# Optimization experiments

Measured on AMD Instinct MI355X. Metric: run time of the kernel, lower is better.

## Reference

```python
import jax, jax.numpy as jnp
import numpy as np
import math

D = 256      # d_model
HEADS = 8
PTS = 4      # num_points
L = 6        # num_layers
FF = 1024    # dim_feedforward
B = 8
HS, WS = 100, 100  # feature map -> N = 10000
HD = D // HEADS


def setup_inputs() -> dict:
    key = jax.random.key(0)
    ks = jax.random.split(key, 8)
    w = lambda k, shape, s: jax.random.normal(k, shape, jnp.float32) * s
    z = lambda *shape: jnp.zeros(shape, jnp.float32)
    return {
        "src": jax.random.normal(ks[0], (B, HS * WS, D), jnp.float32),
        "Wv": w(ks[1], (L, D, D), 0.02), "bv": z(L, D),
        "Woff": w(ks[2], (L, D, HEADS * PTS * 2), 0.01), "boff": z(L, HEADS * PTS * 2),
        "Wa": w(ks[3], (L, D, HEADS * PTS), 0.02), "ba": z(L, HEADS * PTS),
        "Wo": w(ks[4], (L, D, D), 0.02), "bo": z(L, D),
        "W1": w(ks[5], (L, D, FF), 0.02), "b1": z(L, FF),
        "W2": w(ks[6], (L, FF, D), 0.02), "b2": z(L, D),
        "g1": jnp.ones((L, D)), "be1": z(L, D),
        "g2": jnp.ones((L, D)), "be2": z(L, D),
        "H": HS, "W": WS,
    }


def pos_encoding_2d(d_model, H, W):
    # standard 2D sine encoding: first half of channels encode y, second half x
    half = d_model // 2
    freqs = jnp.exp(-math.log(10000.0) * jnp.arange(0, half, 2, dtype=jnp.float32) / half)
    ya = jnp.arange(H, dtype=jnp.float32)[:, None] * freqs[None, :]
    xa = jnp.arange(W, dtype=jnp.float32)[:, None] * freqs[None, :]
    pe_y = jnp.stack([jnp.sin(ya), jnp.cos(ya)], -1).reshape(H, half)
    pe_x = jnp.stack([jnp.sin(xa), jnp.cos(xa)], -1).reshape(W, half)
    pe = jnp.concatenate([
        jnp.broadcast_to(pe_y[:, None, :], (H, W, half)),
        jnp.broadcast_to(pe_x[None, :, :], (H, W, half))], -1)
    return pe.reshape(H * W, d_model)


def layer_norm(x, g, b, eps=1e-5):
    m = x.mean(-1, keepdims=True)
    v = ((x - m) ** 2).mean(-1, keepdims=True)
    return (x - m) * jax.lax.rsqrt(v + eps) * g + b


def deform_attn(q, Wv, bv, Woff, boff, Wa, ba, Wo, bo, H, W):
    # single-scale Deformable-DETR attention; q: [B, N, D], N = H*W
    Bq, N, _ = q.shape
    v = (q @ Wv + bv).reshape(Bq, N, HEADS, HD)
    off = (q @ Woff + boff).reshape(Bq, N, HEADS, PTS, 2)          # (dx, dy) in pixels
    attn = jax.nn.softmax((q @ Wa + ba).reshape(Bq, N, HEADS, PTS), axis=-1)
    # reference points: normalized grid cell centers
    ys, xs = jnp.meshgrid(jnp.arange(H, dtype=jnp.float32),
                          jnp.arange(W, dtype=jnp.float32), indexing='ij')
    ref = jnp.stack([(xs.reshape(-1) + 0.5) / W, (ys.reshape(-1) + 0.5) / H], -1)  # [N,2]
    loc = ref[None, :, None, None, :] + off / jnp.array([W, H], jnp.float32)       # [B,N,h,P,2]
    # pixel coords, align_corners=False; border padding via clamping
    px = loc[..., 0] * W - 0.5
    py = loc[..., 1] * H - 0.5
    x0 = jnp.floor(px); y0 = jnp.floor(py)
    wx = px - x0; wy = py - y0
    x0i = jnp.clip(x0.astype(jnp.int32), 0, W - 1); x1i = jnp.clip(x0i + 1, 0, W - 1)
    y0i = jnp.clip(y0.astype(jnp.int32), 0, H - 1); y1i = jnp.clip(y0i + 1, 0, H - 1)
    vbh = v.transpose(0, 2, 1, 3).reshape(Bq * HEADS, N, HD)       # [B*h, N, hd]
    flat = lambda yi, xi: (yi * W + xi).transpose(0, 2, 1, 3).reshape(Bq * HEADS, N * PTS)
    gather = jax.vmap(lambda val, idx: val[idx])                   # [B*h, N*P, hd]
    wxr = wx.transpose(0, 2, 1, 3).reshape(Bq * HEADS, N * PTS, 1)
    wyr = wy.transpose(0, 2, 1, 3).reshape(Bq * HEADS, N * PTS, 1)
    s = (gather(vbh, flat(y0i, x0i)) * (1 - wxr) * (1 - wyr)
         + gather(vbh, flat(y0i, x1i)) * wxr * (1 - wyr)
         + gather(vbh, flat(y1i, x0i)) * (1 - wxr) * wyr
         + gather(vbh, flat(y1i, x1i)) * wxr * wyr)
    s = s.reshape(Bq, HEADS, N, PTS, HD)
    out = jnp.einsum('bhnp,bhnpd->bhnd', attn.transpose(0, 2, 1, 3), s)
    out = out.transpose(0, 2, 1, 3).reshape(Bq, N, D)
    return out @ Wo + bo


def reference(src, Wv, bv, Woff, boff, Wa, ba, Wo, bo, W1, b1, W2, b2,
              g1, be1, g2, be2, H, W):
    x = src + pos_encoding_2d(D, H, W)[None]
    for i in range(L):
        a = deform_attn(x, Wv[i], bv[i], Woff[i], boff[i], Wa[i], ba[i], Wo[i], bo[i], H, W)
        x = layer_norm(x + a, g1[i], be1[i])
        h = jax.nn.gelu(x @ W1[i] + b1[i], approximate=False)
        x = layer_norm(x + (h @ W2[i] + b2[i]), g2[i], be2[i])
    return x
```

## Files before the change

### kernel.cpp

```cpp
#include <hip/hip_runtime.h>
#include <hip/hip_bf16.h>
#include <math.h>

#define Bq   8
#define NPix 10000
#define HH   100
#define WW   100
#define Dm   256
#define NH   8
#define HD   32
#define PTS  4
#define FFd  1024
#define Lnum 6
#define Mrows (Bq * NPix)

typedef short bf16x8 __attribute__((ext_vector_type(8)));
typedef short short4v __attribute__((ext_vector_type(4)));
typedef float f32x4 __attribute__((ext_vector_type(4)));

__device__ __forceinline__ float bf2f(unsigned short u) {
    return __uint_as_float(((unsigned)u) << 16);
}
__device__ __forceinline__ unsigned short f2bf(float f) {
    unsigned x = __float_as_uint(f);
    return (unsigned short)((x + 0x7fffu + ((x >> 16) & 1u)) >> 16);
}

__global__ __launch_bounds__(256) void pos_add_kernel(
    const float* __restrict__ src, float* __restrict__ x, short* __restrict__ xb)
{
    int idx = blockIdx.x * 256 + threadIdx.x;
    int c = idx & (Dm - 1);
    int n = (idx >> 8) % NPix;
    int cc = c;
    float coord;
    if (c < 128) { coord = (float)(n / WW); }
    else         { coord = (float)(n % WW); cc = c - 128; }
    int j = cc >> 1;
    float f = __expf(-logf(10000.0f) * (2.0f * (float)j) / 128.0f);
    float arg = coord * f;
    float pe = (cc & 1) ? cosf(arg) : sinf(arg);
    float val = src[idx] + pe;
    x[idx] = val;
    xb[idx] = (short)f2bf(val);
}

__global__ __launch_bounds__(256) void repack_kernel(
    const float* __restrict__ W, short* __restrict__ Wt,
    int K, int N, int outLstride, int nOff)
{
    __shared__ float t[64][65];
    int l  = blockIdx.z;
    int k0 = blockIdx.y * 64, n0 = blockIdx.x * 64;
    const float* Wl = W + (size_t)l * K * N;
    for (int i = threadIdx.x; i < 64 * 64; i += 256) {
        int kk = i >> 6, nn = i & 63;
        float val = 0.0f;
        if (k0 + kk < K && n0 + nn < N) val = Wl[(size_t)(k0 + kk) * N + (n0 + nn)];
        t[kk][nn] = val;
    }
    __syncthreads();
    for (int i = threadIdx.x; i < 64 * 64; i += 256) {
        int nn = i >> 6, kk = i & 63;
        if (n0 + nn < N && k0 + kk < K)
            Wt[(size_t)l * outLstride + (size_t)(nOff + n0 + nn) * K + (k0 + kk)]
                = (short)f2bf(t[kk][nn]);
    }
}

__global__ void bcat_kernel(const float* __restrict__ bv,
                            const float* __restrict__ boff,
                            const float* __restrict__ ba,
                            float* __restrict__ bcat)
{
    int l = blockIdx.x, c = threadIdx.x;
    float v;
    if (c < 256)      v = bv[l * 256 + c];
    else if (c < 320) v = boff[l * 64 + (c - 256)];
    else              v = ba[l * 32 + (c - 320)];
    bcat[l * 352 + c] = v;
}

template<bool GELU, int MODE>
__global__ __launch_bounds__(256) void gemm_mfma_kernel(
    const short* __restrict__ A, const short* __restrict__ Bt,
    const float* __restrict__ bias, void* __restrict__ Cv,
    float* __restrict__ C2,
    int M, int K, int Nc, int ldc)
{
    __shared__ short As[128 * 64];
    __shared__ short Bs[128 * 64];
    const int tid = threadIdx.x;

    int nwg  = gridDim.x * gridDim.y;
    int orig = blockIdx.y * gridDim.x + blockIdx.x;
    int xcd  = orig & 7, pos = orig >> 3;
    int q = nwg >> 3, r = nwg & 7;
    int flat = (xcd < r ? xcd * (q + 1) : r * (q + 1) + (xcd - r) * q) + pos;
    const int bm = (flat / gridDim.x) * 128;
    const int bn = (flat % gridDim.x) * 128;

    const int w = tid >> 6, l = tid & 63;
    const int wr = (w >> 1) * 64, wc = (w & 1) * 64;

    f32x4 acc[4][4];
    #pragma unroll
    for (int m = 0; m < 4; ++m)
        #pragma unroll
        for (int n = 0; n < 4; ++n)
            #pragma unroll
            for (int j = 0; j < 4; ++j) acc[m][n][j] = 0.0f;

    const int rl = tid >> 3;
    const int cl = tid & 7;
    const int lr = l & 15, lq = l >> 4;

    for (int k0 = 0; k0 < K; k0 += 64) {
        #pragma unroll
        for (int p = 0; p < 4; ++p) {
            int row = p * 32 + rl;
            int sc  = cl ^ (row & 7);
            int ga  = bm + row; if (ga > M - 1) ga = M - 1;
            __builtin_amdgcn_global_load_lds((const void*)(A + (size_t)ga * K + k0 + sc * 8),
                (void*)&As[(p * 32 + w * 8) * 64], 16, 0, 0);
            int gb = bn + row; if (gb > Nc - 1) gb = Nc - 1;
            __builtin_amdgcn_global_load_lds((const void*)(Bt + (size_t)gb * K + k0 + sc * 8),
                (void*)&Bs[(p * 32 + w * 8) * 64], 16, 0, 0);
        }
        __syncthreads();

        #pragma unroll
        for (int ks = 0; ks < 2; ++ks) {
            bf16x8 af[4], bfr[4];
            #pragma unroll
            for (int m = 0; m < 4; ++m) {
                int row = wr + m * 16 + lr;
                int ch  = (ks * 4 + lq) ^ (row & 7);
                af[m] = *(const bf16x8*)&As[row * 64 + ch * 8];
            }
            #pragma unroll
            for (int n = 0; n < 4; ++n) {
                int row = wc + n * 16 + lr;
                int ch  = (ks * 4 + lq) ^ (row & 7);
                bfr[n] = *(const bf16x8*)&Bs[row * 64 + ch * 8];
            }
            #pragma unroll
            for (int m = 0; m < 4; ++m)
                #pragma unroll
                for (int n = 0; n < 4; ++n)
                    acc[m][n] = __builtin_amdgcn_mfma_f32_16x16x32_bf16(
                        af[m], bfr[n], acc[m][n], 0, 0, 0);
        }
        __syncthreads();
    }

    #pragma unroll
    for (int m = 0; m < 4; ++m) {
        int row0 = bm + wr + m * 16 + lq * 4;
        #pragma unroll
        for (int n = 0; n < 4; ++n) {
            int col = bn + wc + n * 16 + lr;
            if (col >= Nc) continue;
            float bi = bias[col];
            #pragma unroll
            for (int j = 0; j < 4; ++j) {
                int rr = row0 + j;
                if (rr >= M) continue;
                float val = acc[m][n][j] + bi;
                if (GELU)
                    val = 0.5f * val * (1.0f + erff(val * 0.70710678118654752f));
                if (MODE == 1) {
                    ((short*)Cv)[(size_t)rr * ldc + col] = (short)f2bf(val);
                } else {
                    if (col < 256)
                        ((short*)Cv)[(size_t)rr * 256 + col] = (short)f2bf(val);
                    else
                        C2[(size_t)rr * 96 + (col - 256)] = val;
                }
            }
        }
    }
}

__global__ __launch_bounds__(256) void gemm_ln_kernel(
    const short* __restrict__ A, const short* __restrict__ Bt,
    const float* __restrict__ bias,
    const float* __restrict__ gw, const float* __restrict__ bw,
    float* __restrict__ x, short* __restrict__ xb,
    int M, int K)
{
    __shared__ short As[64 * 64];
    __shared__ short Bs[256 * 64];
    const int tid = threadIdx.x;
    const int bm = blockIdx.x * 64;
    const int w = tid >> 6, l = tid & 63;
    const int rl = tid >> 3, cl = tid & 7;
    const int lr = l & 15, lq = l >> 4;

    f32x4 acc[16];
    #pragma unroll
    for (int n = 0; n < 16; ++n)
        #pragma unroll
        for (int j = 0; j < 4; ++j) acc[n][j] = 0.0f;

    for (int k0 = 0; k0 < K; k0 += 64) {
        #pragma unroll
        for (int p = 0; p < 2; ++p) {
            int row = p * 32 + rl;
            int sc  = cl ^ (row & 7);
            int ga  = bm + row; if (ga > M - 1) ga = M - 1;
            __builtin_amdgcn_global_load_lds((const void*)(A + (size_t)ga * K + k0 + sc * 8),
                (void*)&As[(p * 32 + w * 8) * 64], 16, 0, 0);
        }
        #pragma unroll
        for (int p = 0; p < 8; ++p) {
            int row = p * 32 + rl;
            int sc  = cl ^ (row & 7);
            __builtin_amdgcn_global_load_lds((const void*)(Bt + (size_t)row * K + k0 + sc * 8),
                (void*)&Bs[(p * 32 + w * 8) * 64], 16, 0, 0);
        }
        __syncthreads();

        #pragma unroll
        for (int ks = 0; ks < 2; ++ks) {
            int arow = w * 16 + lr;
            bf16x8 af = *(const bf16x8*)&As[arow * 64 + (((ks * 4 + lq) ^ (arow & 7))) * 8];
            #pragma unroll
            for (int hb = 0; hb < 2; ++hb) {
                bf16x8 bfr[8];
                #pragma unroll
                for (int i = 0; i < 8; ++i) {
                    int brow = (hb * 8 + i) * 16 + lr;
                    bfr[i] = *(const bf16x8*)&Bs[brow * 64 + (((ks * 4 + lq) ^ (brow & 7))) * 8];
                }
                #pragma unroll
                for (int i = 0; i < 8; ++i)
                    acc[hb * 8 + i] = __builtin_amdgcn_mfma_f32_16x16x32_bf16(
                        af, bfr[i], acc[hb * 8 + i], 0, 0, 0);
            }
        }
        __syncthreads();
    }

    float bi[16];
    #pragma unroll
    for (int n = 0; n < 16; ++n) bi[n] = bias[n * 16 + lr];

    #pragma unroll
    for (int j = 0; j < 4; ++j) {
        int rr = bm + w * 16 + lq * 4 + j;
        if (rr < M) {
            float tmp[16];
            float sum = 0.0f;
            #pragma unroll
            for (int n = 0; n < 16; ++n) {
                int c = n * 16 + lr;
                float val = acc[n][j] + bi[n] + x[(size_t)rr * 256 + c];
                tmp[n] = val;
                sum += val;
            }
            #pragma unroll
            for (int o = 8; o >= 1; o >>= 1) sum += __shfl_xor(sum, o);
            float mean = sum * (1.0f / 256.0f);
            float vs = 0.0f;
            #pragma unroll
            for (int n = 0; n < 16; ++n) {
                float d = tmp[n] - mean;
                vs += d * d;
            }
            #pragma unroll
            for (int o = 8; o >= 1; o >>= 1) vs += __shfl_xor(vs, o);
            float rstd = rsqrtf(vs * (1.0f / 256.0f) + 1e-5f);
            #pragma unroll
            for (int n = 0; n < 16; ++n) {
                int c = n * 16 + lr;
                float ov = (tmp[n] - mean) * rstd * gw[c] + bw[c];
                x[(size_t)rr * 256 + c] = ov;
                xb[(size_t)rr * 256 + c] = (short)f2bf(ov);
            }
        }
    }
}

__global__ __launch_bounds__(256) void deform_attn_kernel(
    const short* __restrict__ v, const float* __restrict__ comb,
    short* __restrict__ outs)
{
    int g  = blockIdx.x * 16 + (threadIdx.x >> 4);
    int d2 = threadIdx.x & 15;
    int bn = g >> 3, h = g & 7;
    int n  = bn % NPix;
    int row = n / WW, col = n % WW;
    int base_v = (bn / NPix) * NPix;

    const float* cb = comb + (size_t)bn * 96;
    float l0 = cb[64 + h * 4 + 0], l1 = cb[64 + h * 4 + 1];
    float l2 = cb[64 + h * 4 + 2], l3 = cb[64 + h * 4 + 3];
    float mx = fmaxf(fmaxf(l0, l1), fmaxf(l2, l3));
    float e0 = __expf(l0 - mx), e1 = __expf(l1 - mx);
    float e2 = __expf(l2 - mx), e3 = __expf(l3 - mx);
    float inv = 1.0f / (e0 + e1 + e2 + e3);
    float aw[4] = {e0 * inv, e1 * inv, e2 * inv, e3 * inv};

    float acc0 = 0.0f, acc1 = 0.0f;
    size_t chb = (size_t)h * HD + d2 * 2;
    #pragma unroll
    for (int p = 0; p < 4; ++p) {
        float dx = cb[h * 8 + p * 2 + 0];
        float dy = cb[h * 8 + p * 2 + 1];
        float px = (float)col + dx;
        float py = (float)row + dy;
        float x0f = floorf(px), y0f = floorf(py);
        float wx = px - x0f, wy = py - y0f;
        int x0i = min(max((int)x0f, 0), WW - 1);
        int y0i = min(max((int)y0f, 0), HH - 1);
        int x1i = min(x0i + 1, WW - 1);
        int y1i = min(y0i + 1, HH - 1);
        unsigned u00 = *(const unsigned*)&v[(size_t)(base_v + y0i * WW + x0i) * Dm + chb];
        unsigned u01 = *(const unsigned*)&v[(size_t)(base_v + y0i * WW + x1i) * Dm + chb];
        unsigned u10 = *(const unsigned*)&v[(size_t)(base_v + y1i * WW + x0i) * Dm + chb];
        unsigned u11 = *(const unsigned*)&v[(size_t)(base_v + y1i * WW + x1i) * Dm + chb];
        float w00 = (1.0f - wx) * (1.0f - wy), w01 = wx * (1.0f - wy);
        float w10 = (1.0f - wx) * wy,          w11 = wx * wy;
        float s0 = bf2f((unsigned short)u00) * w00 + bf2f((unsigned short)u01) * w01
                 + bf2f((unsigned short)u10) * w10 + bf2f((unsigned short)u11) * w11;
        float s1 = bf2f((unsigned short)(u00 >> 16)) * w00 + bf2f((unsigned short)(u01 >> 16)) * w01
                 + bf2f((unsigned short)(u10 >> 16)) * w10 + bf2f((unsigned short)(u11 >> 16)) * w11;
        acc0 = fmaf(aw[p], s0, acc0);
        acc1 = fmaf(aw[p], s1, acc1);
    }
    unsigned outw = (unsigned)f2bf(acc0) | ((unsigned)f2bf(acc1) << 16);
    *(unsigned*)&outs[(size_t)bn * Dm + chb] = outw;
}

extern "C" void kernel_launch(void* const* d_in, const int* in_sizes, int n_in,
                              void* d_out, int out_size, void* d_ws, size_t ws_size,
                              hipStream_t stream)
{
    const float* src  = (const float*)d_in[0];
    const float* Wv   = (const float*)d_in[1];
    const float* bv   = (const float*)d_in[2];
    const float* Woff = (const float*)d_in[3];
    const float* boff = (const float*)d_in[4];
    const float* Wa   = (const float*)d_in[5];
    const float* ba   = (const float*)d_in[6];
    const float* Wo   = (const float*)d_in[7];
    const float* bo   = (const float*)d_in[8];
    const float* W1   = (const float*)d_in[9];
    const float* b1   = (const float*)d_in[10];
    const float* W2   = (const float*)d_in[11];
    const float* b2   = (const float*)d_in[12];
    const float* g1   = (const float*)d_in[13];
    const float* be1  = (const float*)d_in[14];
    const float* g2   = (const float*)d_in[15];
    const float* be2  = (const float*)d_in[16];

    float* x = (float*)d_out;

    char* cur = (char*)d_ws;
    auto take = [&](size_t bytes) { char* p = cur; cur += (bytes + 255) & ~(size_t)255; return p; };
    short* WcatT = (short*)take((size_t)Lnum * 352 * Dm * 2);
    short* WoT   = (short*)take((size_t)Lnum * Dm * Dm * 2);
    short* W1T   = (short*)take((size_t)Lnum * Dm * FFd * 2);
    short* W2T   = (short*)take((size_t)Lnum * FFd * Dm * 2);
    float* bcat  = (float*)take((size_t)Lnum * 352 * 4);
    short* xb    = (short*)take((size_t)Mrows * Dm * 2);
    size_t fixedB = (size_t)(cur - (char*)d_ws);

    const size_t perRowB = 512 + 512 + 384 + 2048;
    int k = 8;
    while (k > 1 && fixedB + (size_t)k * NPix * perRowB > ws_size) k >>= 1;
    if (fixedB + (size_t)k * NPix * perRowB > ws_size) return;
    const int CM = k * NPix;
    const int nChunks = Bq / k;

    short* v    = (short*)take((size_t)CM * Dm * 2);
    short* sbuf = (short*)take((size_t)CM * Dm * 2);
    float* comb = (float*)take((size_t)CM * 96 * 4);
    short* h    = (short*)take((size_t)CM * FFd * 2);

    repack_kernel<<<dim3(4, 4, Lnum),  256, 0, stream>>>(Wv,   WcatT, Dm,  Dm,  352 * Dm,   0);
    repack_kernel<<<dim3(1, 4, Lnum),  256, 0, stream>>>(Woff, WcatT, Dm,  64,  352 * Dm, 256);
    repack_kernel<<<dim3(1, 4, Lnum),  256, 0, stream>>>(Wa,   WcatT, Dm,  32,  352 * Dm, 320);
    repack_kernel<<<dim3(4, 4, Lnum),  256, 0, stream>>>(Wo,   WoT,   Dm,  Dm,  Dm * Dm,    0);
    repack_kernel<<<dim3(16, 4, Lnum), 256, 0, stream>>>(W1,   W1T,   Dm,  FFd, Dm * FFd,   0);
    repack_kernel<<<dim3(4, 16, Lnum), 256, 0, stream>>>(W2,   W2T,   FFd, Dm,  FFd * Dm,   0);
    bcat_kernel<<<Lnum, 352, 0, stream>>>(bv, boff, ba, bcat);

    pos_add_kernel<<<Mrows, 256, 0, stream>>>(src, x, xb);

    const int gy   = (CM + 127) / 128;
    const int gLN  = (CM + 63) / 64;

    for (int l = 0; l < Lnum; ++l) {
        const short* WcatT_l = WcatT + (size_t)l * 352 * Dm;
        const short* WoT_l   = WoT   + (size_t)l * Dm * Dm;
        const short* W1T_l   = W1T   + (size_t)l * Dm * FFd;
        const short* W2T_l   = W2T   + (size_t)l * FFd * Dm;

        for (int c = 0; c < nChunks; ++c) {
            size_t rowOff = (size_t)c * CM;
            float* xc  = x  + rowOff * Dm;
            short* xbc = xb + rowOff * Dm;

            gemm_mfma_kernel<false, 2><<<dim3(3, gy), 256, 0, stream>>>(
                xbc, WcatT_l, bcat + l * 352, v, comb, CM, Dm, 352, 0);
            deform_attn_kernel<<<CM / 2, 256, 0, stream>>>(v, comb, sbuf);
            gemm_ln_kernel<<<gLN, 256, 0, stream>>>(
                sbuf, WoT_l, bo + l * Dm, g1 + l * Dm, be1 + l * Dm, xc, xbc, CM, Dm);
            gemm_mfma_kernel<true, 1><<<dim3(8, gy), 256, 0, stream>>>(
                xbc, W1T_l, b1 + l * FFd, h, nullptr, CM, Dm, FFd, FFd);
            gemm_ln_kernel<<<gLN, 256, 0, stream>>>(
                h, W2T_l, b2 + l * Dm, g2 + l * Dm, be2 + l * Dm, xc, xbc, CM, FFd);
        }
    }
}
```

Before: 2.706 ms.

## Fuse FFN up-projection, GELU, down-projection and LayerNorm into one kernel

Replaces the separate W1 GEMM+GELU kernel and the W2 GEMM+LayerNorm kernel with a single kernel. Each 64-row block computes the 1024-wide hidden activation in four 256-column strips kept in LDS and immediately accumulates them into the W2 output, so the bf16 hidden tensor never goes to global memory. This removes the hidden-buffer write and read and one launch per chunk, and frees workspace for larger chunks. The cost is heavy LDS use (about 96KB per block), which limits occupancy, and weight tiles reloaded per 64-row block with little overlap between loads and MFMA.

```diff
diff --git a/kernel.cpp b/kernel.cpp
--- a/kernel.cpp
+++ b/kernel.cpp
@@ -245,6 +245,180 @@
     float bi[16];
     #pragma unroll
     for (int n = 0; n < 16; ++n) bi[n] = bias[n * 16 + lr];
+
+    #pragma unroll
+    for (int j = 0; j < 4; ++j) {
+        int rr = bm + w * 16 + lq * 4 + j;
+        if (rr < M) {
+            float tmp[16];
+            float sum = 0.0f;
+            #pragma unroll
+            for (int n = 0; n < 16; ++n) {
+                int c = n * 16 + lr;
+                float val = acc[n][j] + bi[n] + x[(size_t)rr * 256 + c];
+                tmp[n] = val;
+                sum += val;
+            }
+            #pragma unroll
+            for (int o = 8; o >= 1; o >>= 1) sum += __shfl_xor(sum, o);
+            float mean = sum * (1.0f / 256.0f);
+            float vs = 0.0f;
+            #pragma unroll
+            for (int n = 0; n < 16; ++n) {
+                float d = tmp[n] - mean;
+                vs += d * d;
+            }
+            #pragma unroll
+            for (int o = 8; o >= 1; o >>= 1) vs += __shfl_xor(vs, o);
+            float rstd = rsqrtf(vs * (1.0f / 256.0f) + 1e-5f);
+            #pragma unroll
+            for (int n = 0; n < 16; ++n) {
+                int c = n * 16 + lr;
+                float ov = (tmp[n] - mean) * rstd * gw[c] + bw[c];
+                x[(size_t)rr * 256 + c] = ov;
+                xb[(size_t)rr * 256 + c] = (short)f2bf(ov);
+            }
+        }
+    }
+}
+
+__global__ __launch_bounds__(256) void ffn_ln_kernel(
+    const short* __restrict__ A,
+    const short* __restrict__ W1T,
+    const short* __restrict__ W2T,
+    const float* __restrict__ b1, const float* __restrict__ b2,
+    const float* __restrict__ gw, const float* __restrict__ bw,
+    float* __restrict__ x, short* __restrict__ xb,
+    int M)
+{
+    __shared__ short As[64 * 256];
+    __shared__ short hL[64 * 256];
+    __shared__ short Wst[256 * 64];
+    const int tid = threadIdx.x;
+    const int bm = blockIdx.x * 64;
+    const int w = tid >> 6, l = tid & 63;
+    const int lr = l & 15, lq = l >> 4;
+
+    #pragma unroll
+    for (int p = 0; p < 8; ++p) {
+        int s = p * 256 + tid;
+        int row = s >> 5, cs = s & 31;
+        int c = cs ^ (row & 7);
+        int ga = bm + row; if (ga > M - 1) ga = M - 1;
+        __builtin_amdgcn_global_load_lds((const void*)(A + (size_t)ga * 256 + c * 8),
+            (void*)&As[(size_t)(p * 256 + w * 64) * 8], 16, 0, 0);
+    }
+
+    f32x4 acc[16];
+    #pragma unroll
+    for (int n = 0; n < 16; ++n)
+        #pragma unroll
+        for (int j = 0; j < 4; ++j) acc[n][j] = 0.0f;
+
+    const int srow = tid >> 3;
+
+    for (int strip = 0; strip < 4; ++strip) {
+        f32x4 hacc[16];
+        #pragma unroll
+        for (int n = 0; n < 16; ++n)
+            #pragma unroll
+            for (int j = 0; j < 4; ++j) hacc[n][j] = 0.0f;
+
+        const short* W1s = W1T + (size_t)(strip * 256) * 256;
+        for (int kc = 0; kc < 4; ++kc) {
+            __syncthreads();
+            #pragma unroll
+            for (int p = 0; p < 8; ++p) {
+                int s = p * 256 + tid;
+                int row = s >> 3, cs = s & 7;
+                int c = cs ^ (row & 7);
+                __builtin_amdgcn_global_load_lds(
+                    (const void*)(W1s + (size_t)row * 256 + kc * 64 + c * 8),
+                    (void*)&Wst[(size_t)(p * 256 + w * 64) * 8], 16, 0, 0);
+            }
+            __syncthreads();
+
+            #pragma unroll
+            for (int ks = 0; ks < 2; ++ks) {
+                int arow = w * 16 + lr;
+                int ac = (kc * 8 + ks * 4 + lq) ^ (arow & 7);
+                bf16x8 xf = *(const bf16x8*)&As[arow * 256 + ac * 8];
+                #pragma unroll
+                for (int hb = 0; hb < 2; ++hb) {
+                    bf16x8 wf[8];
+                    #pragma unroll
+                    for (int i = 0; i < 8; ++i) {
+                        int wrow = (hb * 8 + i) * 16 + lr;
+                        wf[i] = *(const bf16x8*)&Wst[wrow * 64 + (((ks * 4 + lq) ^ (wrow & 7))) * 8];
+                    }
+                    #pragma unroll
+                    for (int i = 0; i < 8; ++i)
+                        hacc[hb * 8 + i] = __builtin_amdgcn_mfma_f32_16x16x32_bf16(
+                            wf[i], xf, hacc[hb * 8 + i], 0, 0, 0);
+                }
+            }
+        }
+
+        {
+            int hrow = w * 16 + lr;
+            #pragma unroll
+            for (int n = 0; n < 16; ++n) {
+                float4 b1v = *(const float4*)(b1 + strip * 256 + n * 16 + lq * 4);
+                float o0 = hacc[n][0] + b1v.x;
+                float o1 = hacc[n][1] + b1v.y;
+                float o2 = hacc[n][2] + b1v.z;
+                float o3 = hacc[n][3] + b1v.w;
+                o0 = 0.5f * o0 * (1.0f + erff(o0 * 0.70710678118654752f));
+                o1 = 0.5f * o1 * (1.0f + erff(o1 * 0.70710678118654752f));
+                o2 = 0.5f * o2 * (1.0f + erff(o2 * 0.70710678118654752f));
+                o3 = 0.5f * o3 * (1.0f + erff(o3 * 0.70710678118654752f));
+                unsigned lo = (unsigned)f2bf(o0) | ((unsigned)f2bf(o1) << 16);
+                unsigned hi = (unsigned)f2bf(o2) | ((unsigned)f2bf(o3) << 16);
+                int col = n * 16 + lq * 4;
+                int slot = (col >> 3) ^ (hrow & 7);
+                unsigned long long val = ((unsigned long long)hi << 32) | (unsigned long long)lo;
+                *(unsigned long long*)((char*)hL + (size_t)hrow * 512 + slot * 16 + (col & 7) * 2) = val;
+            }
+        }
+
+        for (int kc = 0; kc < 4; ++kc) {
+            __syncthreads();
+            #pragma unroll
+            for (int p = 0; p < 8; ++p) {
+                int s = p * 256 + tid;
+                int row = s >> 3, cs = s & 7;
+                int c = cs ^ (row & 7);
+                __builtin_amdgcn_global_load_lds(
+                    (const void*)(W2T + (size_t)row * 1024 + strip * 256 + kc * 64 + c * 8),
+                    (void*)&Wst[(size_t)(p * 256 + w * 64) * 8], 16, 0, 0);
+            }
+            __syncthreads();
+
+            #pragma unroll
+            for (int ks = 0; ks < 2; ++ks) {
+                int hrow = w * 16 + lr;
+                int hc = (kc * 8 + ks * 4 + lq) ^ (hrow & 7);
+                bf16x8 hf = *(const bf16x8*)&hL[hrow * 256 + hc * 8];
+                #pragma unroll
+                for (int hb = 0; hb < 2; ++hb) {
+                    bf16x8 wf[8];
+                    #pragma unroll
+                    for (int i = 0; i < 8; ++i) {
+                        int wrow = (hb * 8 + i) * 16 + lr;
+                        wf[i] = *(const bf16x8*)&Wst[wrow * 64 + (((ks * 4 + lq) ^ (wrow & 7))) * 8];
+                    }
+                    #pragma unroll
+                    for (int i = 0; i < 8; ++i)
+                        acc[hb * 8 + i] = __builtin_amdgcn_mfma_f32_16x16x32_bf16(
+                            hf, wf[i], acc[hb * 8 + i], 0, 0, 0);
+                }
+            }
+        }
+    }
+
+    float bi[16];
+    #pragma unroll
+    for (int n = 0; n < 16; ++n) bi[n] = b2[n * 16 + lr];
 
     #pragma unroll
     for (int j = 0; j < 4; ++j) {
@@ -367,7 +541,7 @@
     short* xb    = (short*)take((size_t)Mrows * Dm * 2);
     size_t fixedB = (size_t)(cur - (char*)d_ws);
 
-    const size_t perRowB = 512 + 512 + 384 + 2048;
+    const size_t perRowB = 512 + 512 + 384;
     int k = 8;
     while (k > 1 && fixedB + (size_t)k * NPix * perRowB > ws_size) k >>= 1;
     if (fixedB + (size_t)k * NPix * perRowB > ws_size) return;
@@ -377,7 +551,6 @@
     short* v    = (short*)take((size_t)CM * Dm * 2);
     short* sbuf = (short*)take((size_t)CM * Dm * 2);
     float* comb = (float*)take((size_t)CM * 96 * 4);
-    short* h    = (short*)take((size_t)CM * FFd * 2);
 
     repack_kernel<<<dim3(4, 4, Lnum),  256, 0, stream>>>(Wv,   WcatT, Dm,  Dm,  352 * Dm,   0);
     repack_kernel<<<dim3(1, 4, Lnum),  256, 0, stream>>>(Woff, WcatT, Dm,  64,  352 * Dm, 256);
@@ -389,8 +562,8 @@
 
     pos_add_kernel<<<Mrows, 256, 0, stream>>>(src, x, xb);
 
-    const int gy   = (CM + 127) / 128;
-    const int gLN  = (CM + 63) / 64;
+    const int gy  = (CM + 127) / 128;
+    const int gLN = (CM + 63) / 64;
 
     for (int l = 0; l < Lnum; ++l) {
         const short* WcatT_l = WcatT + (size_t)l * 352 * Dm;
@@ -408,10 +581,9 @@
             deform_attn_kernel<<<CM / 2, 256, 0, stream>>>(v, comb, sbuf);
             gemm_ln_kernel<<<gLN, 256, 0, stream>>>(
                 sbuf, WoT_l, bo + l * Dm, g1 + l * Dm, be1 + l * Dm, xc, xbc, CM, Dm);
-            gemm_mfma_kernel<true, 1><<<dim3(8, gy), 256, 0, stream>>>(
-                xbc, W1T_l, b1 + l * FFd, h, nullptr, CM, Dm, FFd, FFd);
-            gemm_ln_kernel<<<gLN, 256, 0, stream>>>(
-                h, W2T_l, b2 + l * Dm, g2 + l * Dm, be2 + l * Dm, xc, xbc, CM, FFd);
-        }
-    }
-}
+            ffn_ln_kernel<<<gLN, 256, 0, stream>>>(
+                xbc, W1T_l, W2T_l, b1 + l * FFd, b2 + l * Dm,
+                g2 + l * Dm, be2 + l * Dm, xc, xbc, CM);
+        }
+    }
+}
```

Result: slower. 3.035 ms (+12.2%).

## Replace W1/Wo/W2 GEMMs with persistent double-buffered 256x256 tile kernel

Applied to the files above, without the earlier changes.

Adds a persistent 512-thread GEMM kernel with 256x256 output tiles, double-buffered LDS staging that prefetches the next k-chunk or next tile, and XCD-aware tile assignment. It serves the Wo and W2 projections with a fused residual+LayerNorm epilogue that reduces across waves through shared memory, and the W1 projection with a GELU epilogue. The aim is more operand reuse per tile and load/compute overlap. In exchange it uses 128KB+ of LDS and large accumulator register arrays, which limits occupancy and can leave many CUs idle when there are few 256-row tiles.

```diff
diff --git a/kernel.cpp b/kernel.cpp
--- a/kernel.cpp
+++ b/kernel.cpp
@@ -15,7 +15,6 @@
 #define Mrows (Bq * NPix)
 
 typedef short bf16x8 __attribute__((ext_vector_type(8)));
-typedef short short4v __attribute__((ext_vector_type(4)));
 typedef float f32x4 __attribute__((ext_vector_type(4)));
 
 __device__ __forceinline__ float bf2f(unsigned short u) {
@@ -81,12 +80,11 @@
     bcat[l * 352 + c] = v;
 }
 
-template<bool GELU, int MODE>
 __global__ __launch_bounds__(256) void gemm_mfma_kernel(
     const short* __restrict__ A, const short* __restrict__ Bt,
-    const float* __restrict__ bias, void* __restrict__ Cv,
+    const float* __restrict__ bias, short* __restrict__ Cv,
     float* __restrict__ C2,
-    int M, int K, int Nc, int ldc)
+    int M, int K, int Nc)
 {
     __shared__ short As[128 * 64];
     __shared__ short Bs[128 * 64];
@@ -167,116 +165,206 @@
                 int rr = row0 + j;
                 if (rr >= M) continue;
                 float val = acc[m][n][j] + bi;
-                if (GELU)
-                    val = 0.5f * val * (1.0f + erff(val * 0.70710678118654752f));
-                if (MODE == 1) {
-                    ((short*)Cv)[(size_t)rr * ldc + col] = (short)f2bf(val);
-                } else {
-                    if (col < 256)
-                        ((short*)Cv)[(size_t)rr * 256 + col] = (short)f2bf(val);
-                    else
-                        C2[(size_t)rr * 96 + (col - 256)] = val;
-                }
-            }
-        }
-    }
-}
-
-__global__ __launch_bounds__(256) void gemm_ln_kernel(
+                if (col < 256)
+                    Cv[(size_t)rr * 256 + col] = (short)f2bf(val);
+                else
+                    C2[(size_t)rr * 96 + (col - 256)] = val;
+            }
+        }
+    }
+}
+
+template<int EPI>
+__global__ __launch_bounds__(512, 2) void gemm2_kernel(
     const short* __restrict__ A, const short* __restrict__ Bt,
     const float* __restrict__ bias,
+    short* __restrict__ C, int ldc,
+    float* __restrict__ x, short* __restrict__ xb,
     const float* __restrict__ gw, const float* __restrict__ bw,
-    float* __restrict__ x, short* __restrict__ xb,
-    int M, int K)
-{
-    __shared__ short As[64 * 64];
-    __shared__ short Bs[256 * 64];
+    int M, int K, int Nc, int nTilesM, int nTilesN)
+{
+    __shared__ short As[2][256 * 64];
+    __shared__ short Bs[2][256 * 64];
+    __shared__ float sredS[4][256];
+    __shared__ float sredM[256];
+    __shared__ float sredR[256];
+
     const int tid = threadIdx.x;
-    const int bm = blockIdx.x * 64;
-    const int w = tid >> 6, l = tid & 63;
-    const int rl = tid >> 3, cl = tid & 7;
-    const int lr = l & 15, lq = l >> 4;
-
-    f32x4 acc[16];
-    #pragma unroll
-    for (int n = 0; n < 16; ++n)
+    const int w   = tid >> 6;
+    const int l   = tid & 63;
+    const int lr  = l & 15, lq = l >> 4;
+    const int wr  = (w >> 2) * 128;
+    const int wcg = w & 3;
+    const int wc  = wcg * 64;
+
+    const int nT = nTilesM * nTilesN;
+    const int kIters = K >> 6;
+
+    const int nwg = gridDim.x;
+    {
+    }
+    int orig = blockIdx.x;
+    int xcd = orig & 7, pos = orig >> 3;
+    int q8 = nwg >> 3, r8 = nwg & 7;
+    int b0 = (xcd < r8 ? xcd * (q8 + 1) : r8 * (q8 + 1) + (xcd - r8) * q8) + pos;
+
+    auto stage = [&](int buf, int t, int kc) {
+        int tm = t / nTilesN, tn = t - tm * nTilesN;
         #pragma unroll
-        for (int j = 0; j < 4; ++j) acc[n][j] = 0.0f;
-
-    for (int k0 = 0; k0 < K; k0 += 64) {
+        for (int p = 0; p < 4; ++p) {
+            int s = p * 512 + tid;
+            int row = s >> 3, cs = s & 7;
+            int c = cs ^ (row & 7);
+            int ga = tm * 256 + row; if (ga > M - 1) ga = M - 1;
+            __builtin_amdgcn_global_load_lds(
+                (const void*)(A + (size_t)ga * K + kc * 64 + c * 8),
+                (void*)&As[buf][(p * 512 + w * 64) * 8], 16, 0, 0);
+            int gb = tn * 256 + row;
+            __builtin_amdgcn_global_load_lds(
+                (const void*)(Bt + (size_t)gb * K + kc * 64 + c * 8),
+                (void*)&Bs[buf][(p * 512 + w * 64) * 8], 16, 0, 0);
+        }
+    };
+
+    f32x4 acc[8][4];
+    int cur = 0;
+    int t = b0;
+    if (t < nT) stage(0, t, 0);
+
+    for (; t < nT; t += nwg) {
+        const int tm = t / nTilesN, tn = t - tm * nTilesN;
+
         #pragma unroll
-        for (int p = 0; p < 2; ++p) {
-            int row = p * 32 + rl;
-            int sc  = cl ^ (row & 7);
-            int ga  = bm + row; if (ga > M - 1) ga = M - 1;
-            __builtin_amdgcn_global_load_lds((const void*)(A + (size_t)ga * K + k0 + sc * 8),
-                (void*)&As[(p * 32 + w * 8) * 64], 16, 0, 0);
-        }
-        #pragma unroll
-        for (int p = 0; p < 8; ++p) {
-            int row = p * 32 + rl;
-            int sc  = cl ^ (row & 7);
-            __builtin_amdgcn_global_load_lds((const void*)(Bt + (size_t)row * K + k0 + sc * 8),
-                (void*)&Bs[(p * 32 + w * 8) * 64], 16, 0, 0);
-        }
-        __syncthreads();
-
-        #pragma unroll
-        for (int ks = 0; ks < 2; ++ks) {
-            int arow = w * 16 + lr;
-            bf16x8 af = *(const bf16x8*)&As[arow * 64 + (((ks * 4 + lq) ^ (arow & 7))) * 8];
-            #pragma unroll
-            for (int hb = 0; hb < 2; ++hb) {
-                bf16x8 bfr[8];
-                #pragma unroll
-                for (int i = 0; i < 8; ++i) {
-                    int brow = (hb * 8 + i) * 16 + lr;
-                    bfr[i] = *(const bf16x8*)&Bs[brow * 64 + (((ks * 4 + lq) ^ (brow & 7))) * 8];
+        for (int m = 0; m < 8; ++m)
+            #pragma unroll
+            for (int n = 0; n < 4; ++n)
+                #pragma unroll
+                for (int j = 0; j < 4; ++j) acc[m][n][j] = 0.0f;
+
+        for (int kc = 0; kc < kIters; ++kc) {
+            __syncthreads();
+            int nt2 = t, nk = kc + 1;
+            if (nk == kIters) { nt2 = t + nwg; nk = 0; }
+            if (nt2 < nT) stage(cur ^ 1, nt2, nk);
+
+            #pragma unroll
+            for (int ks = 0; ks < 2; ++ks) {
+                bf16x8 af[8], bfr[4];
+                #pragma unroll
+                for (int m = 0; m < 8; ++m) {
+                    int row = wr + m * 16 + lr;
+                    int ch  = (ks * 4 + lq) ^ (row & 7);
+                    af[m] = *(const bf16x8*)&As[cur][row * 64 + ch * 8];
                 }
                 #pragma unroll
-                for (int i = 0; i < 8; ++i)
-                    acc[hb * 8 + i] = __builtin_amdgcn_mfma_f32_16x16x32_bf16(
-                        af, bfr[i], acc[hb * 8 + i], 0, 0, 0);
-            }
-        }
-        __syncthreads();
-    }
-
-    float bi[16];
-    #pragma unroll
-    for (int n = 0; n < 16; ++n) bi[n] = bias[n * 16 + lr];
-
-    #pragma unroll
-    for (int j = 0; j < 4; ++j) {
-        int rr = bm + w * 16 + lq * 4 + j;
-        if (rr < M) {
-            float tmp[16];
-            float sum = 0.0f;
-            #pragma unroll
-            for (int n = 0; n < 16; ++n) {
-                int c = n * 16 + lr;
-                float val = acc[n][j] + bi[n] + x[(size_t)rr * 256 + c];
-                tmp[n] = val;
-                sum += val;
-            }
-            #pragma unroll
-            for (int o = 8; o >= 1; o >>= 1) sum += __shfl_xor(sum, o);
-            float mean = sum * (1.0f / 256.0f);
-            float vs = 0.0f;
-            #pragma unroll
-            for (int n = 0; n < 16; ++n) {
-                float d = tmp[n] - mean;
-                vs += d * d;
-            }
-            #pragma unroll
-            for (int o = 8; o >= 1; o >>= 1) vs += __shfl_xor(vs, o);
-            float rstd = rsqrtf(vs * (1.0f / 256.0f) + 1e-5f);
-            #pragma unroll
-            for (int n = 0; n < 16; ++n) {
-                int c = n * 16 + lr;
-                float ov = (tmp[n] - mean) * rstd * gw[c] + bw[c];
-                x[(size_t)rr * 256 + c] = ov;
-                xb[(size_t)rr * 256 + c] = (short)f2bf(ov);
+                for (int n = 0; n < 4; ++n) {
+                    int row = wc + n * 16 + lr;
+                    int ch  = (ks * 4 + lq) ^ (row & 7);
+                    bfr[n] = *(const bf16x8*)&Bs[cur][row * 64 + ch * 8];
+                }
+                #pragma unroll
+                for (int m = 0; m < 8; ++m)
+                    #pragma unroll
+                    for (int n = 0; n < 4; ++n)
+                        acc[m][n] = __builtin_amdgcn_mfma_f32_16x16x32_bf16(
+                            af[m], bfr[n], acc[m][n], 0, 0, 0);
+            }
+            cur ^= 1;
+        }
+
+        if (EPI == 0) {
+            #pragma unroll
+            for (int m = 0; m < 8; ++m) {
+                int row0 = tm * 256 + wr + m * 16 + lq * 4;
+                #pragma unroll
+                for (int n = 0; n < 4; ++n) {
+                    int col = tn * 256 + wc + n * 16 + lr;
+                    float bi = bias[col];
+                    #pragma unroll
+                    for (int j = 0; j < 4; ++j) {
+                        int rr = row0 + j;
+                        if (rr >= M) continue;
+                        float val = acc[m][n][j] + bi;
+                        val = 0.5f * val * (1.0f + erff(val * 0.70710678118654752f));
+                        C[(size_t)rr * ldc + col] = (short)f2bf(val);
+                    }
+                }
+            }
+        } else {
+            float bi[4];
+            #pragma unroll
+            for (int n = 0; n < 4; ++n) bi[n] = bias[wc + n * 16 + lr];
+
+            #pragma unroll
+            for (int m = 0; m < 8; ++m) {
+                #pragma unroll
+                for (int j = 0; j < 4; ++j) {
+                    int rr = tm * 256 + wr + m * 16 + lq * 4 + j;
+                    int rc = rr > M - 1 ? M - 1 : rr;
+                    float s = 0.0f;
+                    #pragma unroll
+                    for (int n = 0; n < 4; ++n) {
+                        int col = wc + n * 16 + lr;
+                        float val = acc[m][n][j] + bi[n] + x[(size_t)rc * 256 + col];
+                        acc[m][n][j] = val;
+                        s += val;
+                    }
+                    #pragma unroll
+                    for (int o = 8; o >= 1; o >>= 1) s += __shfl_xor(s, o);
+                    if (lr == 0) sredS[wcg][wr + m * 16 + lq * 4 + j] = s;
+                }
+            }
+            __syncthreads();
+            if (tid < 256) {
+                float s = sredS[0][tid] + sredS[1][tid] + sredS[2][tid] + sredS[3][tid];
+                sredM[tid] = s * (1.0f / 256.0f);
+            }
+            __syncthreads();
+            #pragma unroll
+            for (int m = 0; m < 8; ++m) {
+                #pragma unroll
+                for (int j = 0; j < 4; ++j) {
+                    float mean = sredM[wr + m * 16 + lq * 4 + j];
+                    float qsum = 0.0f;
+                    #pragma unroll
+                    for (int n = 0; n < 4; ++n) {
+                        float d = acc[m][n][j] - mean;
+                        qsum += d * d;
+                    }
+                    #pragma unroll
+                    for (int o = 8; o >= 1; o >>= 1) qsum += __shfl_xor(qsum, o);
+                    if (lr == 0) sredS[wcg][wr + m * 16 + lq * 4 + j] = qsum;
+                }
+            }
+            __syncthreads();
+            if (tid < 256) {
+                float s = sredS[0][tid] + sredS[1][tid] + sredS[2][tid] + sredS[3][tid];
+                sredR[tid] = rsqrtf(s * (1.0f / 256.0f) + 1e-5f);
+            }
+            __syncthreads();
+            float gwv[4], bwv[4];
+            #pragma unroll
+            for (int n = 0; n < 4; ++n) {
+                int col = wc + n * 16 + lr;
+                gwv[n] = gw[col]; bwv[n] = bw[col];
+            }
+            #pragma unroll
+            for (int m = 0; m < 8; ++m) {
+                #pragma unroll
+                for (int j = 0; j < 4; ++j) {
+                    int rloc = wr + m * 16 + lq * 4 + j;
+                    int rr = tm * 256 + rloc;
+                    if (rr >= M) continue;
+                    float mean = sredM[rloc];
+                    float rstd = sredR[rloc];
+                    #pragma unroll
+                    for (int n = 0; n < 4; ++n) {
+                        int col = wc + n * 16 + lr;
+                        float ov = (acc[m][n][j] - mean) * rstd * gwv[n] + bwv[n];
+                        x[(size_t)rr * 256 + col] = ov;
+                        xb[(size_t)rr * 256 + col] = (short)f2bf(ov);
+                    }
+                }
             }
         }
     }
@@ -389,8 +477,10 @@
 
     pos_add_kernel<<<Mrows, 256, 0, stream>>>(src, x, xb);
 
-    const int gy   = (CM + 127) / 128;
-    const int gLN  = (CM + 63) / 64;
+    const int gy128 = (CM + 127) / 128;
+    const int nTm   = (CM + 255) / 256;
+    const int gW1   = min(256, nTm * 4);
+    const int gLN   = min(256, nTm);
 
     for (int l = 0; l < Lnum; ++l) {
         const short* WcatT_l = WcatT + (size_t)l * 352 * Dm;
@@ -403,15 +493,21 @@
             float* xc  = x  + rowOff * Dm;
             short* xbc = xb + rowOff * Dm;
 
-            gemm_mfma_kernel<false, 2><<<dim3(3, gy), 256, 0, stream>>>(
-                xbc, WcatT_l, bcat + l * 352, v, comb, CM, Dm, 352, 0);
+            gemm_mfma_kernel<<<dim3(3, gy128), 256, 0, stream>>>(
+                xbc, WcatT_l, bcat + l * 352, v, comb, CM, Dm, 352);
             deform_attn_kernel<<<CM / 2, 256, 0, stream>>>(v, comb, sbuf);
-            gemm_ln_kernel<<<gLN, 256, 0, stream>>>(
-                sbuf, WoT_l, bo + l * Dm, g1 + l * Dm, be1 + l * Dm, xc, xbc, CM, Dm);
-            gemm_mfma_kernel<true, 1><<<dim3(8, gy), 256, 0, stream>>>(
-                xbc, W1T_l, b1 + l * FFd, h, nullptr, CM, Dm, FFd, FFd);
-            gemm_ln_kernel<<<gLN, 256, 0, stream>>>(
-                h, W2T_l, b2 + l * Dm, g2 + l * Dm, be2 + l * Dm, xc, xbc, CM, FFd);
-        }
-    }
-}
+            gemm2_kernel<1><<<gLN, 512, 0, stream>>>(
+                sbuf, WoT_l, bo + l * Dm, nullptr, 0,
+                xc, xbc, g1 + l * Dm, be1 + l * Dm,
+                CM, Dm, Dm, nTm, 1);
+            gemm2_kernel<0><<<gW1, 512, 0, stream>>>(
+                xbc, W1T_l, b1 + l * FFd, h, FFd,
+                nullptr, nullptr, nullptr, nullptr,
+                CM, Dm, FFd, nTm, 4);
+            gemm2_kernel<1><<<gLN, 512, 0, stream>>>(
+                h, W2T_l, b2 + l * Dm, nullptr, 0,
+                xc, xbc, g2 + l * Dm, be2 + l * Dm,
+                CM, FFd, Dm, nTm, 1);
+        }
+    }
+}
```

Result: slower. 3.935 ms (+45.4%).
